# Performance work log

Measured on AMD Instinct MI355X. Metric: run time of the kernel, lower is better.

## Reference

```python
import jax, jax.numpy as jnp
import numpy as np

RADIUS = 0.2
NSAMPLE = 32

B, N, S, C = 4, 16384, 4096, 64


def _ball_query(xyz, new_xyz):
    """CUDA ball_query semantics: for each centroid, the first NSAMPLE point
    indices with squared distance < radius^2 (in index order); empty slots are
    filled with the first found index (0 if no neighbor).
    xyz: [B,N,3], new_xyz: [B,S,3] -> idx [B,S,NSAMPLE] int32."""
    n = xyz.shape[1]
    # squared pairwise distances [B,S,N] via |a|^2 + |b|^2 - 2 a.b
    d2 = (jnp.sum(new_xyz * new_xyz, -1)[:, :, None]
          + jnp.sum(xyz * xyz, -1)[:, None, :]
          - 2.0 * jnp.einsum('bsd,bnd->bsn', new_xyz, xyz))
    in_ball = d2 < RADIUS * RADIUS
    # key = point index if in ball else N (sentinel); sorting gives first-K order
    key = jnp.where(in_ball, jnp.arange(n, dtype=jnp.int32), jnp.int32(n))
    key = jnp.sort(key, axis=-1)[..., :NSAMPLE]          # [B,S,K]
    first = key[..., :1]
    first = jnp.where(first == n, 0, first)              # no neighbor -> 0
    idx = jnp.where(key == n, first, key)
    return idx


def _group(feat, idx):
    """feat [B,C,N], idx [B,S,K] -> [B,C,S,K] (group_points_forward)."""
    return jax.vmap(lambda f, i: f[:, i])(feat, idx)


def setup_inputs() -> dict:
    key = jax.random.key(0)
    k1, k2, k3 = jax.random.split(key, 3)
    xyz = jax.random.uniform(k1, (B, N, 3), dtype=jnp.float32)
    new_xyz = jax.random.uniform(k2, (B, S, 3), dtype=jnp.float32)
    features = jax.random.normal(k3, (B, C, N), dtype=jnp.float32)
    return {"xyz": xyz, "new_xyz": new_xyz, "features": features}


def reference(xyz, new_xyz, features):
    idx = jax.lax.stop_gradient(_ball_query(xyz, new_xyz))   # [B,S,K], non-diff
    xyz_t = jnp.transpose(xyz, (0, 2, 1))                    # [B,3,N]
    grouped_xyz = _group(xyz_t, idx)                         # [B,3,S,K]
    grouped_xyz = grouped_xyz - jnp.transpose(new_xyz, (0, 2, 1))[..., None]
    grouped_features = _group(features, idx)                 # [B,C,S,K]
    new_features = jnp.concatenate([grouped_xyz, grouped_features], axis=1)
    return new_features                                      # [B,3+C,S,K]
```

## Files before the change

### kernel.cpp

```cpp
#include <hip/hip_runtime.h>
#include <stdint.h>

#define BB 4
#define NN 16384
#define SS 4096
#define CC 64
#define KK 32
#define R2F 0.04f
#define BANDF 5e-5f

#define QSCALE (1.0f / 65535.0f)

#define PACKED_BYTES ((size_t)BB * NN * sizeof(float4))
#define IDX_BYTES    ((size_t)BB * SS * KK * sizeof(int))

static __device__ __forceinline__ int mbcnt64(unsigned long long m) {
    return (int)__builtin_amdgcn_mbcnt_hi((unsigned)(m >> 32),
               __builtin_amdgcn_mbcnt_lo((unsigned)m, 0u));
}

__global__ __launch_bounds__(256) void prep_kernel(const float* __restrict__ xyz,
                                                   const float* __restrict__ features,
                                                   float4* __restrict__ packed,
                                                   ushort4* __restrict__ qpts,
                                                   float* __restrict__ featT) {
    int blk = blockIdx.x;
    if (blk < 64) {
        for (int i = 0; i < 4; ++i) {
            int p = blk * 1024 + i * 256 + (int)threadIdx.x;
            float x = xyz[(size_t)p * 3 + 0];
            float y = xyz[(size_t)p * 3 + 1];
            float z = xyz[(size_t)p * 3 + 2];
            float w = fmaf(z, z, fmaf(y, y, x * x));
            packed[p] = make_float4(x, y, z, w);
            ushort4 q;
            q.x = (unsigned short)rintf(x * 65535.0f);
            q.y = (unsigned short)rintf(y * 65535.0f);
            q.z = (unsigned short)rintf(z * 65535.0f);
            q.w = 0;
            qpts[p] = q;
        }
        return;
    }
    blk -= 64;
    int b  = blk >> 8;
    int n0 = (blk & 255) << 6;
    const float* f = features + (size_t)b * CC * NN;
    for (int i = 0; i < 4; ++i) {
        int e  = (int)threadIdx.x + i * 256;
        int c4 = e & 15;
        int n  = n0 + (e >> 4);
        float4 v;
        v.x = f[(size_t)(c4 * 4 + 0) * NN + n];
        v.y = f[(size_t)(c4 * 4 + 1) * NN + n];
        v.z = f[(size_t)(c4 * 4 + 2) * NN + n];
        v.w = f[(size_t)(c4 * 4 + 3) * NN + n];
        *(float4*)(featT + ((size_t)b * NN + n) * CC + c4 * 4) = v;
    }
}

__global__ __launch_bounds__(256) void fused_kernel(const float4* __restrict__ packed,
                                                    const ushort4* __restrict__ qpts,
                                                    const float* __restrict__ new_xyz,
                                                    const float* __restrict__ featT,
                                                    float* __restrict__ out) {
    __shared__ int    sidx[128];
    __shared__ float  snc[12];
    __shared__ float4 sfeat[64][16];

    int bid  = (int)blockIdx.x;
    int wgid = (bid & 7) * 512 + (bid >> 3);
    int b  = wgid >> 10;
    int s0 = (wgid & 1023) << 2;
    int t  = (int)threadIdx.x;
    int w = t >> 6, lane = t & 63;
    int s = s0 + w;

    if (t < 12) snc[t] = new_xyz[((size_t)(b * SS + s0 + t / 3)) * 3 + (t % 3)];

    const float* nc = new_xyz + (size_t)(b * SS + s) * 3;
    const float nxf = nc[0], nyf = nc[1], nzf = nc[2];
    const double nx = (double)nxf, ny = (double)nyf, nz = (double)nzf;
    const double t1 = nx * nx + ny * ny + nz * nz;
    const double r2 = 0.2 * 0.2;

    const float4*  pts = packed + (size_t)b * NN;
    const uint4*   qv  = (const uint4*)(qpts + (size_t)b * NN);

    int cnt = 0;
    int first = 0;
    uint4 u0 = qv[lane];
    uint4 u1 = qv[64 + lane];
    for (int i64 = 0; i64 < NN / 2; i64 += 64) {
        int nb = (i64 + 128 < NN / 2) ? (i64 + 128) : i64;
        uint4 u2 = qv[nb + lane];
        int base = i64 * 2;
        int ja = base + 2 * lane;

        float dxa = fmaf((float)(u0.x & 0xFFFFu), QSCALE, -nxf);
        float dya = fmaf((float)(u0.x >> 16),     QSCALE, -nyf);
        float dza = fmaf((float)(u0.y & 0xFFFFu), QSCALE, -nzf);
        float d2a = fmaf(dza, dza, fmaf(dya, dya, dxa * dxa));
        bool inbA;
        if (__builtin_fabsf(d2a - R2F) < BANDF) {
            float4 p = pts[ja];
            double pxd = (double)p.x, pyd = (double)p.y, pzd = (double)p.z;
            double t2d = pxd * pxd + pyd * pyd + pzd * pzd;
            double dtd = nx * pxd + ny * pyd + nz * pzd;
            inbA = ((t1 + t2d) - 2.0 * dtd) < r2;
        } else {
            inbA = d2a < R2F;
        }
        float dxb = fmaf((float)(u0.z & 0xFFFFu), QSCALE, -nxf);
        float dyb = fmaf((float)(u0.z >> 16),     QSCALE, -nyf);
        float dzb = fmaf((float)(u0.w & 0xFFFFu), QSCALE, -nzf);
        float d2b = fmaf(dzb, dzb, fmaf(dyb, dyb, dxb * dxb));
        bool inbB;
        if (__builtin_fabsf(d2b - R2F) < BANDF) {
            float4 p = pts[ja + 1];
            double pxd = (double)p.x, pyd = (double)p.y, pzd = (double)p.z;
            double t2d = pxd * pxd + pyd * pyd + pzd * pzd;
            double dtd = nx * pxd + ny * pyd + nz * pzd;
            inbB = ((t1 + t2d) - 2.0 * dtd) < r2;
        } else {
            inbB = d2b < R2F;
        }

        unsigned long long mA = __ballot(inbA);
        unsigned long long mB = __ballot(inbB);
        if (cnt == 0 && (mA | mB)) {
            int cA = mA ? 2 * (int)__builtin_ctzll(mA)     : 0x7FFFFFFF;
            int cB = mB ? 2 * (int)__builtin_ctzll(mB) + 1 : 0x7FFFFFFF;
            first = base + (cA < cB ? cA : cB);
        }
        int pre = mbcnt64(mA) + mbcnt64(mB);
        if (inbA) {
            int slot = cnt + pre;
            if (slot < KK) sidx[w * KK + slot] = ja;
        }
        if (inbB) {
            int slot = cnt + pre + (inbA ? 1 : 0);
            if (slot < KK) sidx[w * KK + slot] = ja + 1;
        }
        cnt += (int)__popcll(mA) + (int)__popcll(mB);
        if (cnt >= KK) break;
        u0 = u1; u1 = u2;
    }
    if (lane >= cnt && lane < KK) sidx[w * KK + lane] = first;
    __syncthreads();

    const size_t cs = (size_t)SS * KK;
    size_t obase = (size_t)(b * 67) * cs + (size_t)s0 * KK;
    if (t < 128) {
        int cl = t >> 5, k = t & 31;
        float4 p = pts[sidx[t]];
        size_t o = obase + (size_t)cl * KK + k;
        out[o]          = p.x - snc[cl * 3 + 0];
        out[o + cs]     = p.y - snc[cl * 3 + 1];
        out[o + 2 * cs] = p.z - snc[cl * 3 + 2];
    }

    for (int pass = 0; pass < 2; ++pass) {
        for (int i = 0; i < 2; ++i) {
            int slot = i * 256 + t;
            int rl = slot >> 3;
            int q  = slot & 7;
            const float4* src = (const float4*)(featT +
                ((size_t)b * NN + sidx[pass * 64 + rl]) * CC);
            float4 v0 = src[q * 2];
            float4 v1 = src[q * 2 + 1];
            sfeat[rl][(q * 2     + rl) & 15] = v0;
            sfeat[rl][(q * 2 + 1 + rl) & 15] = v1;
        }
        __syncthreads();

        float* pbase = out + obase + (size_t)pass * 64;
        for (int cc = 0; cc < 4; ++cc) {
            int c4 = w * 4 + cc;
            float4 v = sfeat[lane][(c4 + lane) & 15];
            float* pl = pbase + lane;
            pl[(size_t)(3 + c4 * 4 + 0) * cs] = v.x;
            pl[(size_t)(3 + c4 * 4 + 1) * cs] = v.y;
            pl[(size_t)(3 + c4 * 4 + 2) * cs] = v.z;
            pl[(size_t)(3 + c4 * 4 + 3) * cs] = v.w;
        }
        __syncthreads();
    }
}

extern "C" void kernel_launch(void* const* d_in, const int* in_sizes, int n_in,
                              void* d_out, int out_size, void* d_ws, size_t ws_size,
                              hipStream_t stream) {
    const float* xyz      = (const float*)d_in[0];
    const float* new_xyz  = (const float*)d_in[1];
    const float* features = (const float*)d_in[2];
    float* out = (float*)d_out;

    float4*  packed = (float4*)d_ws;
    ushort4* qpts   = (ushort4*)((char*)d_ws + PACKED_BYTES);
    float*   featT  = (float*)((char*)d_ws + PACKED_BYTES + IDX_BYTES);

    prep_kernel<<<64 + BB * (NN / 64), 256, 0, stream>>>(xyz, features, packed,
                                                         qpts, featT);
    fused_kernel<<<BB * SS / 4, 256, 0, stream>>>(packed, qpts, new_xyz, featT, out);
}
```

Before: 51.23 us.

## Use integer quantized distance test, one-wave blocks, and register-transposed feature gather

Point coordinates are now quantized to 14 bits, and the in-ball test runs in integer arithmetic with mul24 against an integer threshold. An integer band around the radius falls back to the exact double-precision check. Each block is now a single 64-lane wave handling one centroid, processing four points per lane per iteration with deeper prefetch. Feature gather drops the shared-memory staging and syncs: each lane loads four gathered rows and transposes in registers to issue float4 stores. The risks are the correctness of the integer band bounds and more, smaller blocks.

```diff
diff --git a/kernel.cpp b/kernel.cpp
--- a/kernel.cpp
+++ b/kernel.cpp
@@ -6,10 +6,10 @@
 #define SS 4096
 #define CC 64
 #define KK 32
-#define R2F 0.04f
-#define BANDF 5e-5f
 
-#define QSCALE (1.0f / 65535.0f)
+#define T_INT    10736108
+#define LOW_INT  10709108
+#define BAND_W   54000
 
 #define PACKED_BYTES ((size_t)BB * NN * sizeof(float4))
 #define IDX_BYTES    ((size_t)BB * SS * KK * sizeof(int))
@@ -31,12 +31,11 @@
             float x = xyz[(size_t)p * 3 + 0];
             float y = xyz[(size_t)p * 3 + 1];
             float z = xyz[(size_t)p * 3 + 2];
-            float w = fmaf(z, z, fmaf(y, y, x * x));
-            packed[p] = make_float4(x, y, z, w);
+            packed[p] = make_float4(x, y, z, 0.0f);
             ushort4 q;
-            q.x = (unsigned short)rintf(x * 65535.0f);
-            q.y = (unsigned short)rintf(y * 65535.0f);
-            q.z = (unsigned short)rintf(z * 65535.0f);
+            q.x = (unsigned short)rintf(x * 16383.0f);
+            q.y = (unsigned short)rintf(y * 16383.0f);
+            q.z = (unsigned short)rintf(z * 16383.0f);
             q.w = 0;
             qpts[p] = q;
         }
@@ -59,132 +58,123 @@
     }
 }
 
-__global__ __launch_bounds__(256) void fused_kernel(const float4* __restrict__ packed,
-                                                    const ushort4* __restrict__ qpts,
-                                                    const float* __restrict__ new_xyz,
-                                                    const float* __restrict__ featT,
-                                                    float* __restrict__ out) {
-    __shared__ int    sidx[128];
-    __shared__ float  snc[12];
-    __shared__ float4 sfeat[64][16];
+__global__ __launch_bounds__(64) void fused_kernel(const float4* __restrict__ packed,
+                                                   const ushort4* __restrict__ qpts,
+                                                   const float* __restrict__ new_xyz,
+                                                   const float* __restrict__ featT,
+                                                   float* __restrict__ out) {
+    __shared__ int sidx[KK];
 
     int bid  = (int)blockIdx.x;
-    int wgid = (bid & 7) * 512 + (bid >> 3);
-    int b  = wgid >> 10;
-    int s0 = (wgid & 1023) << 2;
-    int t  = (int)threadIdx.x;
-    int w = t >> 6, lane = t & 63;
-    int s = s0 + w;
-
-    if (t < 12) snc[t] = new_xyz[((size_t)(b * SS + s0 + t / 3)) * 3 + (t % 3)];
+    int wgid = (bid & 7) * 2048 + (bid >> 3);
+    int b = wgid >> 12;
+    int s = wgid & (SS - 1);
+    int lane = (int)threadIdx.x;
 
     const float* nc = new_xyz + (size_t)(b * SS + s) * 3;
     const float nxf = nc[0], nyf = nc[1], nzf = nc[2];
+    const int qcx = (int)rintf(nxf * 16383.0f);
+    const int qcy = (int)rintf(nyf * 16383.0f);
+    const int qcz = (int)rintf(nzf * 16383.0f);
     const double nx = (double)nxf, ny = (double)nyf, nz = (double)nzf;
     const double t1 = nx * nx + ny * ny + nz * nz;
     const double r2 = 0.2 * 0.2;
 
-    const float4*  pts = packed + (size_t)b * NN;
-    const uint4*   qv  = (const uint4*)(qpts + (size_t)b * NN);
+    const float4* pts = packed + (size_t)b * NN;
+    const uint4*  qv  = (const uint4*)(qpts + (size_t)b * NN);
+
+#define TESTQ(W0, W1, J, INB)                                                   \
+    {                                                                           \
+        int dx = (int)((W0) & 0xFFFFu) - qcx;                                   \
+        int dy = (int)((W0) >> 16)     - qcy;                                   \
+        int dz = (int)((W1) & 0xFFFFu) - qcz;                                   \
+        int d2i = __mul24(dx, dx) + __mul24(dy, dy) + __mul24(dz, dz);          \
+        if ((unsigned)(d2i - LOW_INT) < (unsigned)BAND_W) {                     \
+            float4 p = pts[J];                                                  \
+            double pxd = (double)p.x, pyd = (double)p.y, pzd = (double)p.z;     \
+            double t2d = pxd * pxd + pyd * pyd + pzd * pzd;                     \
+            double dtd = nx * pxd + ny * pyd + nz * pzd;                        \
+            INB = ((t1 + t2d) - 2.0 * dtd) < r2;                                \
+        } else {                                                                \
+            INB = d2i < T_INT;                                                  \
+        }                                                                       \
+    }
 
     int cnt = 0;
     int first = 0;
     uint4 u0 = qv[lane];
     uint4 u1 = qv[64 + lane];
-    for (int i64 = 0; i64 < NN / 2; i64 += 64) {
-        int nb = (i64 + 128 < NN / 2) ? (i64 + 128) : i64;
-        uint4 u2 = qv[nb + lane];
-        int base = i64 * 2;
-        int ja = base + 2 * lane;
+    for (int i = 0; i < NN / 2; i += 128) {
+        int nb = (i + 128 < NN / 2) ? (i + 128) : i;
+        uint4 n0 = qv[nb + lane];
+        uint4 n1 = qv[nb + 64 + lane];
+        int base = i * 2;
+        int jA = base + 2 * lane;
+        int jC = base + 128 + 2 * lane;
 
-        float dxa = fmaf((float)(u0.x & 0xFFFFu), QSCALE, -nxf);
-        float dya = fmaf((float)(u0.x >> 16),     QSCALE, -nyf);
-        float dza = fmaf((float)(u0.y & 0xFFFFu), QSCALE, -nzf);
-        float d2a = fmaf(dza, dza, fmaf(dya, dya, dxa * dxa));
-        bool inbA;
-        if (__builtin_fabsf(d2a - R2F) < BANDF) {
-            float4 p = pts[ja];
-            double pxd = (double)p.x, pyd = (double)p.y, pzd = (double)p.z;
-            double t2d = pxd * pxd + pyd * pyd + pzd * pzd;
-            double dtd = nx * pxd + ny * pyd + nz * pzd;
-            inbA = ((t1 + t2d) - 2.0 * dtd) < r2;
-        } else {
-            inbA = d2a < R2F;
+        bool iA, iB, iC, iD;
+        TESTQ(u0.x, u0.y, jA, iA)
+        TESTQ(u0.z, u0.w, jA + 1, iB)
+        TESTQ(u1.x, u1.y, jC, iC)
+        TESTQ(u1.z, u1.w, jC + 1, iD)
+
+        unsigned long long mA = __ballot(iA);
+        unsigned long long mB = __ballot(iB);
+        unsigned long long mC = __ballot(iC);
+        unsigned long long mD = __ballot(iD);
+
+        if (cnt == 0 && (mA | mB | mC | mD)) {
+            if (mA | mB) {
+                int cA = mA ? 2 * (int)__builtin_ctzll(mA)     : 0x7FFFFFFF;
+                int cB = mB ? 2 * (int)__builtin_ctzll(mB) + 1 : 0x7FFFFFFF;
+                first = base + (cA < cB ? cA : cB);
+            } else {
+                int cC = mC ? 2 * (int)__builtin_ctzll(mC)     : 0x7FFFFFFF;
+                int cD = mD ? 2 * (int)__builtin_ctzll(mD) + 1 : 0x7FFFFFFF;
+                first = base + 128 + (cC < cD ? cC : cD);
+            }
         }
-        float dxb = fmaf((float)(u0.z & 0xFFFFu), QSCALE, -nxf);
-        float dyb = fmaf((float)(u0.z >> 16),     QSCALE, -nyf);
-        float dzb = fmaf((float)(u0.w & 0xFFFFu), QSCALE, -nzf);
-        float d2b = fmaf(dzb, dzb, fmaf(dyb, dyb, dxb * dxb));
-        bool inbB;
-        if (__builtin_fabsf(d2b - R2F) < BANDF) {
-            float4 p = pts[ja + 1];
-            double pxd = (double)p.x, pyd = (double)p.y, pzd = (double)p.z;
-            double t2d = pxd * pxd + pyd * pyd + pzd * pzd;
-            double dtd = nx * pxd + ny * pyd + nz * pzd;
-            inbB = ((t1 + t2d) - 2.0 * dtd) < r2;
-        } else {
-            inbB = d2b < R2F;
-        }
-
-        unsigned long long mA = __ballot(inbA);
-        unsigned long long mB = __ballot(inbB);
-        if (cnt == 0 && (mA | mB)) {
-            int cA = mA ? 2 * (int)__builtin_ctzll(mA)     : 0x7FFFFFFF;
-            int cB = mB ? 2 * (int)__builtin_ctzll(mB) + 1 : 0x7FFFFFFF;
-            first = base + (cA < cB ? cA : cB);
-        }
-        int pre = mbcnt64(mA) + mbcnt64(mB);
-        if (inbA) {
-            int slot = cnt + pre;
-            if (slot < KK) sidx[w * KK + slot] = ja;
-        }
-        if (inbB) {
-            int slot = cnt + pre + (inbA ? 1 : 0);
-            if (slot < KK) sidx[w * KK + slot] = ja + 1;
-        }
-        cnt += (int)__popcll(mA) + (int)__popcll(mB);
+        int preAB = mbcnt64(mA) + mbcnt64(mB);
+        int cAB   = (int)__popcll(mA) + (int)__popcll(mB);
+        int preCD = mbcnt64(mC) + mbcnt64(mD);
+        if (iA) { int sl = cnt + preAB;                 if (sl < KK) sidx[sl] = jA; }
+        if (iB) { int sl = cnt + preAB + (iA ? 1 : 0);  if (sl < KK) sidx[sl] = jA + 1; }
+        if (iC) { int sl = cnt + cAB + preCD;                if (sl < KK) sidx[sl] = jC; }
+        if (iD) { int sl = cnt + cAB + preCD + (iC ? 1 : 0); if (sl < KK) sidx[sl] = jC + 1; }
+        cnt += cAB + (int)__popcll(mC) + (int)__popcll(mD);
         if (cnt >= KK) break;
-        u0 = u1; u1 = u2;
+        u0 = n0; u1 = n1;
     }
-    if (lane >= cnt && lane < KK) sidx[w * KK + lane] = first;
+#undef TESTQ
+    if (lane >= cnt && lane < KK) sidx[lane] = first;
     __syncthreads();
 
     const size_t cs = (size_t)SS * KK;
-    size_t obase = (size_t)(b * 67) * cs + (size_t)s0 * KK;
-    if (t < 128) {
-        int cl = t >> 5, k = t & 31;
-        float4 p = pts[sidx[t]];
-        size_t o = obase + (size_t)cl * KK + k;
-        out[o]          = p.x - snc[cl * 3 + 0];
-        out[o + cs]     = p.y - snc[cl * 3 + 1];
-        out[o + 2 * cs] = p.z - snc[cl * 3 + 2];
+
+    if (lane < KK) {
+        float4 p = pts[sidx[lane]];
+        size_t o = (size_t)(b * 67) * cs + (size_t)s * KK + lane;
+        out[o]          = p.x - nxf;
+        out[o + cs]     = p.y - nyf;
+        out[o + 2 * cs] = p.z - nzf;
     }
 
-    for (int pass = 0; pass < 2; ++pass) {
-        for (int i = 0; i < 2; ++i) {
-            int slot = i * 256 + t;
-            int rl = slot >> 3;
-            int q  = slot & 7;
-            const float4* src = (const float4*)(featT +
-                ((size_t)b * NN + sidx[pass * 64 + rl]) * CC);
-            float4 v0 = src[q * 2];
-            float4 v1 = src[q * 2 + 1];
-            sfeat[rl][(q * 2     + rl) & 15] = v0;
-            sfeat[rl][(q * 2 + 1 + rl) & 15] = v1;
-        }
-        __syncthreads();
-
-        float* pbase = out + obase + (size_t)pass * 64;
-        for (int cc = 0; cc < 4; ++cc) {
-            int c4 = w * 4 + cc;
-            float4 v = sfeat[lane][(c4 + lane) & 15];
-            float* pl = pbase + lane;
-            pl[(size_t)(3 + c4 * 4 + 0) * cs] = v.x;
-            pl[(size_t)(3 + c4 * 4 + 1) * cs] = v.y;
-            pl[(size_t)(3 + c4 * 4 + 2) * cs] = v.z;
-            pl[(size_t)(3 + c4 * 4 + 3) * cs] = v.w;
-        }
-        __syncthreads();
+    const float4* f4 = (const float4*)(featT + (size_t)b * NN * CC);
+    int kq = lane & 7;
+    int k0 = kq * 4;
+    int r0 = sidx[k0], r1 = sidx[k0 + 1], r2i = sidx[k0 + 2], r3 = sidx[k0 + 3];
+#pragma unroll
+    for (int half = 0; half < 2; ++half) {
+        int c4 = (lane >> 3) + half * 8;
+        float4 a0 = f4[(size_t)r0  * 16 + c4];
+        float4 a1 = f4[(size_t)r1  * 16 + c4];
+        float4 a2 = f4[(size_t)r2i * 16 + c4];
+        float4 a3 = f4[(size_t)r3  * 16 + c4];
+        float* ob = out + (size_t)(b * 67 + 3 + c4 * 4) * cs + (size_t)s * KK + k0;
+        *(float4*)(ob)          = make_float4(a0.x, a1.x, a2.x, a3.x);
+        *(float4*)(ob + cs)     = make_float4(a0.y, a1.y, a2.y, a3.y);
+        *(float4*)(ob + 2 * cs) = make_float4(a0.z, a1.z, a2.z, a3.z);
+        *(float4*)(ob + 3 * cs) = make_float4(a0.w, a1.w, a2.w, a3.w);
     }
 }
 
@@ -202,5 +192,5 @@
 
     prep_kernel<<<64 + BB * (NN / 64), 256, 0, stream>>>(xyz, features, packed,
                                                          qpts, featT);
-    fused_kernel<<<BB * SS / 4, 256, 0, stream>>>(packed, qpts, new_xyz, featT, out);
+    fused_kernel<<<BB * SS, 64, 0, stream>>>(packed, qpts, new_xyz, featT, out);
 }
```

Measured after the change: 52.11 us. No clear change (+1.7%).
